# Kernel optimization log

Measured on AMD Instinct MI355X. Metric: run time of the kernel, lower is better.

Reference implementation:

```python
import jax, jax.numpy as jnp
import numpy as np

N_HEADS = 4
M = 16            # n_points (neighbors kept per voxel)
DIST = 4          # manhattan distance threshold
D_MODEL = 128
D_FFN = 256
D_CHL = 64
GRID = 96         # spatial_shape per axis
LN_EPS = 1e-5
BN_EPS = 1e-3


def setup_inputs() -> dict:
    key = jax.random.key(0)
    ks = jax.random.split(key, 24)
    N = 8192
    w = lambda k, s: jax.random.normal(k, s, jnp.float32) * 0.02
    z = lambda d: jnp.zeros((d,), jnp.float32)
    o = lambda d: jnp.ones((d,), jnp.float32)
    return {
        "features": jax.random.normal(ks[0], (N, D_CHL), jnp.float32),
        "coords": jax.random.randint(ks[1], (N, 3), 0, GRID, jnp.int32),
        "pe_w1": w(ks[2], (3, D_MODEL // 2)), "pe_b1": z(D_MODEL // 2),
        "pe_w2": w(ks[3], (D_MODEL // 2, D_MODEL)), "pe_b2": z(D_MODEL),
        "in_w": w(ks[4], (D_CHL, D_MODEL)), "in_b": z(D_MODEL),
        "q_w": w(ks[5], (D_MODEL, D_MODEL)), "q_b": z(D_MODEL),
        "k_w": w(ks[6], (D_MODEL, D_MODEL)), "k_b": z(D_MODEL),
        "v_w": w(ks[7], (D_MODEL, D_MODEL)), "v_b": z(D_MODEL),
        "o_w": w(ks[8], (D_MODEL, D_MODEL)), "o_b": z(D_MODEL),
        "n1_g": o(D_MODEL), "n1_b": z(D_MODEL),
        "l1_w": w(ks[9], (D_MODEL, D_FFN)), "l1_b": z(D_FFN),
        "l2_w": w(ks[10], (D_FFN, D_MODEL)), "l2_b": z(D_MODEL),
        "n3_g": o(D_MODEL), "n3_b": z(D_MODEL),
        "fu_w": w(ks[11], (D_MODEL + D_CHL, D_CHL)), "fu_b": z(D_CHL),
        "bn_g": o(D_CHL), "bn_b": z(D_CHL),
    }


def _layernorm(x, g, b):
    mu = jnp.mean(x, -1, keepdims=True)
    var = jnp.mean(jnp.square(x - mu), -1, keepdims=True)
    return (x - mu) * jax.lax.rsqrt(var + LN_EPS) * g + b


def reference(features, coords, pe_w1, pe_b1, pe_w2, pe_b2, in_w, in_b,
              q_w, q_b, k_w, k_b, v_w, v_b, o_w, o_b, n1_g, n1_b,
              l1_w, l1_b, l2_w, l2_b, n3_g, n3_b, fu_w, fu_b, bn_g, bn_b):
    N = features.shape[0]
    hd = D_MODEL // N_HEADS
    ci = coords.astype(jnp.float32)
    # input projection + dynamic learnable positional encoding
    src = features @ in_w + in_b
    vc = ci / (GRID - 1.0)
    src = src + (jax.nn.relu(vc @ pe_w1 + pe_b1) @ pe_w2 + pe_b2)
    # pairwise manhattan distances; accumulate per coordinate to avoid [N,N,3]
    dist = jnp.zeros((N, N), jnp.float32)
    for d in range(3):
        dist = dist + jnp.abs(ci[:, d, None] - ci[None, :, d])
    dist = jnp.where(dist <= DIST, dist, jnp.inf)
    neg_top, idx = jax.lax.top_k(-dist, M)          # [N, M]
    valid = neg_top != -jnp.inf
    # gather neighbor features; invalid slots are zero (as in torch)
    nb = jnp.where(valid[:, :, None], src[jnp.where(valid, idx, 0)], 0.0)  # [N,M,D]
    # cross-attention: query is neighbor 0 (self). NOTE: faithful raw .view
    # reshape of [N,M,D] -> [N,H,M,hd] (interleaves neighbor/head axes as torch does)
    q = (nb[:, :1] @ q_w + q_b).reshape(N, N_HEADS, 1, hd)
    k = (nb @ k_w + k_b).reshape(N, N_HEADS, M, hd)
    v = (nb @ v_w + v_b).reshape(N, N_HEADS, M, hd)
    scores = jnp.einsum('nhqd,nhkd->nhqk', q, k) / jnp.sqrt(jnp.float32(D_MODEL))
    attn = jax.nn.softmax(scores, axis=-1)
    head_out = jnp.einsum('nhqk,nhkd->nhqd', attn, v).reshape(N, D_MODEL)
    out = head_out @ o_w + o_b
    tgt = _layernorm(src + out, n1_g, n1_b)
    # FFN
    tgt2 = jax.nn.relu(tgt @ l1_w + l1_b) @ l2_w + l2_b
    tgt = _layernorm(tgt + tgt2, n3_g, n3_b)
    # EnhancedFusion: concat -> linear -> batchnorm (train-mode stats) -> relu
    fused = jnp.concatenate([features, tgt], axis=1) @ fu_w + fu_b
    mu = jnp.mean(fused, 0)
    var = jnp.var(fused, 0)
    fused = (fused - mu) * jax.lax.rsqrt(var + BN_EPS) * bn_g + bn_b
    return jax.nn.relu(fused)
```

## Files before the change

### kernel.cpp

```cpp
#include <hip/hip_runtime.h>

#define DEVFN __device__ __forceinline__

DEVFN float relu(float x) { return x < 0.f ? 0.f : x; }

__global__ __launch_bounds__(256, 4) void ka_pre_cst(
    const float* __restrict__ features, const int* __restrict__ coords,
    const float* __restrict__ pe_w1, const float* __restrict__ pe_b1,
    const float* __restrict__ pe_w2, const float* __restrict__ pe_b2,
    const float* __restrict__ in_w, const float* __restrict__ in_b,
    const float* __restrict__ q_w, const float* __restrict__ k_w,
    const float* __restrict__ v_w,
    float* __restrict__ src,
    float* __restrict__ qs, float* __restrict__ ks, float* __restrict__ vs,
    int* __restrict__ nbr, float* __restrict__ bnAcc, int N)
{
    __shared__ __align__(16) float sF[512];
    __shared__ __align__(16) float sH[512];
    __shared__ __align__(16) float S[1024];
    __shared__ int   sC[24];
    __shared__ int cnt[16];
    __shared__ int lst[16 * 64];
    __shared__ int outL[256];

    const int tid = threadIdx.x;
    const int bx = blockIdx.x;
    const int role_nbr = (bx % 3) == 2;

    if (role_nbr) {
        const int nb = bx / 3;
        const int q0 = nb * 16;
        if (nb == 0 && tid < 128) bnAcc[tid] = 0.f;
        if (tid < 16) cnt[tid] = 0;
        outL[tid] = -1;
        __syncthreads();
        int qx[16], qy[16], qz[16];
#pragma unroll
        for (int q = 0; q < 16; ++q) {
            qx[q] = coords[(q0 + q) * 3 + 0];
            qy[q] = coords[(q0 + q) * 3 + 1];
            qz[q] = coords[(q0 + q) * 3 + 2];
        }
        for (int cd = tid; cd < N; cd += 256) {
            int cx = coords[cd * 3 + 0];
            int cy = coords[cd * 3 + 1];
            int cz = coords[cd * 3 + 2];
#pragma unroll
            for (int q = 0; q < 16; ++q) {
                int dx = cx - qx[q]; dx = dx < 0 ? -dx : dx;
                int dy = cy - qy[q]; dy = dy < 0 ? -dy : dy;
                int dz = cz - qz[q]; dz = dz < 0 ? -dz : dz;
                int d = dx + dy + dz;
                if (d <= 4) {
                    int s = atomicAdd(&cnt[q], 1);
                    if (s < 64) lst[q * 64 + s] = (d << 13) | cd;
                }
            }
        }
        __syncthreads();
        {
            const int q = tid >> 4, t = tid & 15;
            int n = cnt[q]; if (n > 64) n = 64;
            for (int e = t; e < n; e += 16) {
                int key = lst[q * 64 + e];
                int rank = 0;
                for (int j = 0; j < n; ++j) rank += (lst[q * 64 + j] < key) ? 1 : 0;
                if (rank < 16) outL[q * 16 + rank] = key & 8191;
            }
        }
        __syncthreads();
        {
            const int q = tid >> 4, t = tid & 15;
            nbr[(q0 + q) * 16 + t] = outL[q * 16 + t];
        }
        return;
    }

    const int sb = (bx / 3) * 2 + (bx % 3);
    const int r0 = sb * 8;
    if (tid < 24) sC[tid] = coords[r0 * 3 + tid];
    for (int i = tid; i < 512; i += 256) sF[i] = features[r0 * 64 + i];
    __syncthreads();
    for (int i = tid; i < 512; i += 256) {
        int r = i >> 6, t = i & 63;
        float v0 = sC[r * 3 + 0] * (1.f / 95.f);
        float v1 = sC[r * 3 + 1] * (1.f / 95.f);
        float v2 = sC[r * 3 + 2] * (1.f / 95.f);
        float h = v0 * pe_w1[t] + v1 * pe_w1[64 + t] + v2 * pe_w1[128 + t] + pe_b1[t];
        sH[i] = relu(h);
    }
    __syncthreads();
    const int c = tid & 127, rh = tid >> 7;
    {
        float acc[4];
        const float base = in_b[c] + pe_b2[c];
#pragma unroll
        for (int r = 0; r < 4; ++r) acc[r] = base;
        const float* wi = in_w + c;
        const float* wp = pe_w2 + c;
        float i0 = wi[0 * 128], i1 = wi[1 * 128], i2 = wi[2 * 128], i3 = wi[3 * 128];
        float p0 = wp[0 * 128], p1 = wp[1 * 128], p2 = wp[2 * 128], p3 = wp[3 * 128];
        for (int j4 = 0; j4 < 16; ++j4) {
            const int jn = ((j4 + 1) & 15) * 4;
            float ni0 = wi[(jn + 0) * 128], ni1 = wi[(jn + 1) * 128];
            float ni2 = wi[(jn + 2) * 128], ni3 = wi[(jn + 3) * 128];
            float np0 = wp[(jn + 0) * 128], np1 = wp[(jn + 1) * 128];
            float np2 = wp[(jn + 2) * 128], np3 = wp[(jn + 3) * 128];
#pragma unroll
            for (int r = 0; r < 4; ++r) {
                const int rr = rh * 4 + r;
                float4 f = *(const float4*)(&sF[rr * 64 + j4 * 4]);
                float4 h = *(const float4*)(&sH[rr * 64 + j4 * 4]);
                acc[r] += f.x * i0 + f.y * i1 + f.z * i2 + f.w * i3
                        + h.x * p0 + h.y * p1 + h.z * p2 + h.w * p3;
            }
            i0 = ni0; i1 = ni1; i2 = ni2; i3 = ni3;
            p0 = np0; p1 = np1; p2 = np2; p3 = np3;
        }
#pragma unroll
        for (int r = 0; r < 4; ++r) {
            src[(r0 + rh * 4 + r) * 128 + c] = acc[r];
            S[(rh * 4 + r) * 128 + c] = acc[r];
        }
    }
    __syncthreads();
    {
        float aq[4], ak[4], av[4];
#pragma unroll
        for (int r = 0; r < 4; ++r) { aq[r] = 0.f; ak[r] = 0.f; av[r] = 0.f; }
        const float* wq = q_w + c;
        const float* wk = k_w + c;
        const float* wv = v_w + c;
        float q0 = wq[0 * 128], q1 = wq[1 * 128], q2 = wq[2 * 128], q3 = wq[3 * 128];
        float k0 = wk[0 * 128], k1 = wk[1 * 128], k2 = wk[2 * 128], k3 = wk[3 * 128];
        float v0 = wv[0 * 128], v1 = wv[1 * 128], v2 = wv[2 * 128], v3 = wv[3 * 128];
        for (int k4 = 0; k4 < 32; ++k4) {
            const int kn = ((k4 + 1) & 31) * 4;
            float nq0 = wq[(kn + 0) * 128], nq1 = wq[(kn + 1) * 128];
            float nq2 = wq[(kn + 2) * 128], nq3 = wq[(kn + 3) * 128];
            float nk0 = wk[(kn + 0) * 128], nk1 = wk[(kn + 1) * 128];
            float nk2 = wk[(kn + 2) * 128], nk3 = wk[(kn + 3) * 128];
            float nv0 = wv[(kn + 0) * 128], nv1 = wv[(kn + 1) * 128];
            float nv2 = wv[(kn + 2) * 128], nv3 = wv[(kn + 3) * 128];
#pragma unroll
            for (int r = 0; r < 4; ++r) {
                float4 s = *(const float4*)(&S[(rh * 4 + r) * 128 + k4 * 4]);
                aq[r] += s.x * q0 + s.y * q1 + s.z * q2 + s.w * q3;
                ak[r] += s.x * k0 + s.y * k1 + s.z * k2 + s.w * k3;
                av[r] += s.x * v0 + s.y * v1 + s.z * v2 + s.w * v3;
            }
            q0 = nq0; q1 = nq1; q2 = nq2; q3 = nq3;
            k0 = nk0; k1 = nk1; k2 = nk2; k3 = nk3;
            v0 = nv0; v1 = nv1; v2 = nv2; v3 = nv3;
        }
#pragma unroll
        for (int r = 0; r < 4; ++r) {
            qs[(r0 + rh * 4 + r) * 128 + c] = aq[r];
            ks[(r0 + rh * 4 + r) * 128 + c] = ak[r];
            vs[(r0 + rh * 4 + r) * 128 + c] = av[r];
        }
    }
}

DEVFN void ln_rows8(float* Cb, const float* __restrict__ g,
                    const float* __restrict__ b, int tid)
{
    const int r = tid >> 5, l = tid & 31;
    float x[4]; float s = 0.f, s2 = 0.f;
#pragma unroll
    for (int i = 0; i < 4; ++i) {
        x[i] = Cb[r * 128 + l * 4 + i];
        s += x[i]; s2 += x[i] * x[i];
    }
#pragma unroll
    for (int o = 1; o < 32; o <<= 1) { s += __shfl_xor(s, o); s2 += __shfl_xor(s2, o); }
    float mu = s * (1.f / 128.f);
    float var = s2 * (1.f / 128.f) - mu * mu;
    float rstd = rsqrtf(var + 1e-5f);
#pragma unroll
    for (int i = 0; i < 4; ++i) {
        int cc = l * 4 + i;
        Cb[r * 128 + cc] = (x[i] - mu) * rstd * g[cc] + b[cc];
    }
}

__global__ __launch_bounds__(256, 4) void k4_main_cst(
    const float* __restrict__ features, const float* __restrict__ src,
    const float* __restrict__ qs, const float* __restrict__ ks, const float* __restrict__ vs,
    const int* __restrict__ nbr,
    const float* __restrict__ q_b, const float* __restrict__ k_b,
    const float* __restrict__ v_b,
    const float* __restrict__ o_w, const float* __restrict__ o_b,
    const float* __restrict__ n1_g, const float* __restrict__ n1_b,
    const float* __restrict__ l1_w, const float* __restrict__ l1_b,
    const float* __restrict__ l2_w, const float* __restrict__ l2_b,
    const float* __restrict__ n3_g, const float* __restrict__ n3_b,
    const float* __restrict__ fu_w, const float* __restrict__ fu_b,
    float* __restrict__ fused, float* __restrict__ bnSum, float* __restrict__ bnSq)
{
    __shared__ __align__(16) float A[1024];
    __shared__ __align__(16) float Bt[1024];
    __shared__ __align__(16) float C[1024];
    __shared__ __align__(16) float Q[1024];
    __shared__ __align__(16) float H[2048];
    __shared__ __align__(16) float SC[512];
    __shared__ __align__(16) float F[512];
    __shared__ __align__(16) float bK[128], bV[128];
    __shared__ int idxL[128];
    const int tid = threadIdx.x;
    const int r0 = blockIdx.x * 8;

    for (int i = tid; i < 1024; i += 256) A[i] = src[r0 * 128 + i];
    for (int i = tid; i < 512; i += 256) F[i] = features[r0 * 64 + i];
    if (tid < 128) {
        idxL[tid] = nbr[r0 * 16 + tid];
        bK[tid] = k_b[tid]; bV[tid] = v_b[tid];
    }
    __syncthreads();
    {
        int r = tid >> 5, cg = tid & 31;
        int i0 = idxL[r * 16];
        float4 qv = make_float4(0.f, 0.f, 0.f, 0.f);
        if (i0 >= 0) qv = *(const float4*)(qs + i0 * 128 + cg * 4);
        float4 qb = *(const float4*)(q_b + cg * 4);
        qv.x += qb.x; qv.y += qb.y; qv.z += qb.z; qv.w += qb.w;
        *(float4*)(&Q[r * 128 + cg * 4]) = qv;
    }
    __syncthreads();

    const int ar = tid >> 5, ah = (tid >> 3) & 3, ag = tid & 7;
    {
#pragma unroll
        for (int jj = 0; jj < 2; ++jj) {
            int j = ag + jj * 8;
            int j4 = j >> 2, ch = j & 3;
            int id = idxL[ar * 16 + ah * 4 + j4];
            float s = 0.f;
#pragma unroll
            for (int c4 = 0; c4 < 8; ++c4) {
                float4 qv = *(const float4*)(&Q[ar * 128 + ah * 32 + c4 * 4]);
                float4 kb = *(const float4*)(&bK[ch * 32 + c4 * 4]);
                float4 kv = make_float4(0.f, 0.f, 0.f, 0.f);
                if (id >= 0) kv = *(const float4*)(ks + id * 128 + ch * 32 + c4 * 4);
                s += qv.x * (kv.x + kb.x) + qv.y * (kv.y + kb.y)
                   + qv.z * (kv.z + kb.z) + qv.w * (kv.w + kb.w);
            }
            SC[ar * 64 + ah * 16 + j] = s * 0.08838834764831845f;
        }
    }
    __syncthreads();

    {
        float p[16];
        float mx = -3.4e38f;
#pragma unroll
        for (int j = 0; j < 16; ++j) { p[j] = SC[ar * 64 + ah * 16 + j]; mx = fmaxf(mx, p[j]); }
        float sum = 0.f;
#pragma unroll
        for (int j = 0; j < 16; ++j) { p[j] = __expf(p[j] - mx); sum += p[j]; }
        float inv = 1.f / sum;
        float4 acc = make_float4(0.f, 0.f, 0.f, 0.f);
#pragma unroll
        for (int j = 0; j < 16; ++j) {
            int j4 = j >> 2, ch = j & 3;
            int id = idxL[ar * 16 + ah * 4 + j4];
            float4 vb = *(const float4*)(&bV[ch * 32 + ag * 4]);
            float4 vv = make_float4(0.f, 0.f, 0.f, 0.f);
            if (id >= 0) vv = *(const float4*)(vs + id * 128 + ch * 32 + ag * 4);
            float w = p[j] * inv;
            acc.x += w * (vv.x + vb.x); acc.y += w * (vv.y + vb.y);
            acc.z += w * (vv.z + vb.z); acc.w += w * (vv.w + vb.w);
        }
        *(float4*)(&Bt[ar * 128 + ah * 32 + ag * 4]) = acc;
    }
    __syncthreads();

    {
        const int c = tid & 127, kh = tid >> 7;
        float acc[8];
#pragma unroll
        for (int r = 0; r < 8; ++r) acc[r] = 0.f;
        const float* wp = o_w + kh * 64 * 128 + c;
        float w0 = wp[0 * 128], w1 = wp[1 * 128], w2 = wp[2 * 128], w3 = wp[3 * 128];
        for (int k4 = 0; k4 < 16; ++k4) {
            const int kn = ((k4 + 1) & 15) * 4;
            float n0 = wp[(kn + 0) * 128], n1 = wp[(kn + 1) * 128];
            float n2 = wp[(kn + 2) * 128], n3 = wp[(kn + 3) * 128];
#pragma unroll
            for (int r = 0; r < 8; ++r) {
                float4 t = *(const float4*)(&Bt[r * 128 + kh * 64 + k4 * 4]);
                acc[r] += t.x * w0 + t.y * w1 + t.z * w2 + t.w * w3;
            }
            w0 = n0; w1 = n1; w2 = n2; w3 = n3;
        }
#pragma unroll
        for (int r = 0; r < 8; ++r) H[kh * 1024 + r * 128 + c] = acc[r];
    }
    __syncthreads();
    for (int i = tid; i < 1024; i += 256) {
        int c = i & 127;
        C[i] = A[i] + o_b[c] + H[i] + H[1024 + i];
    }
    __syncthreads();
    ln_rows8(C, n1_g, n1_b, tid);
    __syncthreads();

    {
        const int f = tid;
        float acc[8];
#pragma unroll
        for (int r = 0; r < 8; ++r) acc[r] = 0.f;
        const float* wp = l1_w + f;
        float w0 = wp[0 * 256], w1 = wp[1 * 256], w2 = wp[2 * 256], w3 = wp[3 * 256];
        for (int k4 = 0; k4 < 32; ++k4) {
            const int kn = ((k4 + 1) & 31) * 4;
            float n0 = wp[(kn + 0) * 256], n1 = wp[(kn + 1) * 256];
            float n2 = wp[(kn + 2) * 256], n3 = wp[(kn + 3) * 256];
#pragma unroll
            for (int r = 0; r < 8; ++r) {
                float4 t = *(const float4*)(&C[r * 128 + k4 * 4]);
                acc[r] += t.x * w0 + t.y * w1 + t.z * w2 + t.w * w3;
            }
            w0 = n0; w1 = n1; w2 = n2; w3 = n3;
        }
        const float bb = l1_b[f];
#pragma unroll
        for (int r = 0; r < 8; ++r) H[r * 256 + f] = relu(acc[r] + bb);
    }
    __syncthreads();

    {
        const int c = tid & 127, kh = tid >> 7;
        float acc[8];
#pragma unroll
        for (int r = 0; r < 8; ++r) acc[r] = 0.f;
        const float* wp = l2_w + kh * 128 * 128 + c;
        float w0 = wp[0 * 128], w1 = wp[1 * 128], w2 = wp[2 * 128], w3 = wp[3 * 128];
        for (int k4 = 0; k4 < 32; ++k4) {
            const int kn = ((k4 + 1) & 31) * 4;
            float n0 = wp[(kn + 0) * 128], n1 = wp[(kn + 1) * 128];
            float n2 = wp[(kn + 2) * 128], n3 = wp[(kn + 3) * 128];
#pragma unroll
            for (int r = 0; r < 8; ++r) {
                float4 t = *(const float4*)(&H[r * 256 + kh * 128 + k4 * 4]);
                acc[r] += t.x * w0 + t.y * w1 + t.z * w2 + t.w * w3;
            }
            w0 = n0; w1 = n1; w2 = n2; w3 = n3;
        }
        float* P = kh ? Bt : A;
#pragma unroll
        for (int r = 0; r < 8; ++r) P[r * 128 + c] = acc[r];
    }
    __syncthreads();
    for (int i = tid; i < 1024; i += 256) {
        int c = i & 127;
        C[i] += l2_b[c] + A[i] + Bt[i];
    }
    __syncthreads();
    ln_rows8(C, n3_g, n3_b, tid);
    __syncthreads();

    {
        const int c = tid & 63, rg = tid >> 6;
        float acc[2];
        const float fb = fu_b[c];
#pragma unroll
        for (int r = 0; r < 2; ++r) acc[r] = fb;
        const float* wA = fu_w + c;
        float w0 = wA[0 * 64], w1 = wA[1 * 64], w2 = wA[2 * 64], w3 = wA[3 * 64];
        for (int j4 = 0; j4 < 16; ++j4) {
            const int jn = ((j4 + 1) & 15) * 4;
            float n0 = wA[(jn + 0) * 64], n1 = wA[(jn + 1) * 64];
            float n2 = wA[(jn + 2) * 64], n3 = wA[(jn + 3) * 64];
#pragma unroll
            for (int r = 0; r < 2; ++r) {
                float4 t = *(const float4*)(&F[(rg * 2 + r) * 64 + j4 * 4]);
                acc[r] += t.x * w0 + t.y * w1 + t.z * w2 + t.w * w3;
            }
            w0 = n0; w1 = n1; w2 = n2; w3 = n3;
        }
        const float* wB = fu_w + 64 * 64 + c;
        w0 = wB[0 * 64]; w1 = wB[1 * 64]; w2 = wB[2 * 64]; w3 = wB[3 * 64];
        for (int j4 = 0; j4 < 32; ++j4) {
            const int jn = ((j4 + 1) & 31) * 4;
            float n0 = wB[(jn + 0) * 64], n1 = wB[(jn + 1) * 64];
            float n2 = wB[(jn + 2) * 64], n3 = wB[(jn + 3) * 64];
#pragma unroll
            for (int r = 0; r < 2; ++r) {
                float4 t = *(const float4*)(&C[(rg * 2 + r) * 128 + j4 * 4]);
                acc[r] += t.x * w0 + t.y * w1 + t.z * w2 + t.w * w3;
            }
            w0 = n0; w1 = n1; w2 = n2; w3 = n3;
        }
#pragma unroll
        for (int r = 0; r < 2; ++r) {
            int row = rg * 2 + r;
            float v = acc[r];
            fused[(r0 + row) * 64 + c] = v;
            H[row * 64 + c] = v;
        }
    }
    __syncthreads();
    if (tid < 64) {
        float s = 0.f, s2 = 0.f;
#pragma unroll
        for (int r = 0; r < 8; ++r) { float x = H[r * 64 + tid]; s += x; s2 += x * x; }
        atomicAdd(&bnSum[tid], s);
        atomicAdd(&bnSq[tid], s2);
    }
}

__global__ __launch_bounds__(256) void k5_bn_cst(
    const float* __restrict__ fused, const float* __restrict__ bnSum,
    const float* __restrict__ bnSq,
    const float* __restrict__ g, const float* __restrict__ b,
    float* __restrict__ out, int N)
{
    const int total = N * 64;
    const float invN = 1.f / (float)N;
    for (int i = blockIdx.x * 256 + threadIdx.x; i < total; i += gridDim.x * 256) {
        int c = i & 63;
        float mu = bnSum[c] * invN;
        float var = bnSq[c] * invN - mu * mu;
        float x = fused[i];
        float y = (x - mu) * rsqrtf(var + 1e-3f) * g[c] + b[c];
        out[i] = relu(y);
    }
}

extern "C" void kernel_launch(void* const* d_in, const int* in_sizes, int n_in,
                              void* d_out, int out_size, void* d_ws, size_t ws_size,
                              hipStream_t stream)
{
    const float* features = (const float*)d_in[0];
    const int*   coords   = (const int*)d_in[1];
    const float* pe_w1 = (const float*)d_in[2];
    const float* pe_b1 = (const float*)d_in[3];
    const float* pe_w2 = (const float*)d_in[4];
    const float* pe_b2 = (const float*)d_in[5];
    const float* in_w  = (const float*)d_in[6];
    const float* in_b  = (const float*)d_in[7];
    const float* q_w   = (const float*)d_in[8];
    const float* q_b   = (const float*)d_in[9];
    const float* k_w   = (const float*)d_in[10];
    const float* k_b   = (const float*)d_in[11];
    const float* v_w   = (const float*)d_in[12];
    const float* v_b   = (const float*)d_in[13];
    const float* o_w   = (const float*)d_in[14];
    const float* o_b   = (const float*)d_in[15];
    const float* n1_g  = (const float*)d_in[16];
    const float* n1_b  = (const float*)d_in[17];
    const float* l1_w  = (const float*)d_in[18];
    const float* l1_b  = (const float*)d_in[19];
    const float* l2_w  = (const float*)d_in[20];
    const float* l2_b  = (const float*)d_in[21];
    const float* n3_g  = (const float*)d_in[22];
    const float* n3_b  = (const float*)d_in[23];
    const float* fu_w  = (const float*)d_in[24];
    const float* fu_b  = (const float*)d_in[25];
    const float* bn_g  = (const float*)d_in[26];
    const float* bn_b  = (const float*)d_in[27];

    const int N = in_sizes[0] / 64;

    float* src   = (float*)d_ws;
    float* qs    = src + (size_t)N * 128;
    float* ks    = qs  + (size_t)N * 128;
    float* vs    = ks  + (size_t)N * 128;
    float* fused = vs  + (size_t)N * 128;
    int*   nbr    = (int*)(fused + (size_t)N * 64);
    float* bnSum  = (float*)(nbr + (size_t)N * 16);
    float* bnSq   = bnSum + 64;

    ka_pre_cst<<<N / 8 + N / 16, 256, 0, stream>>>(features, coords,
                                                   pe_w1, pe_b1, pe_w2, pe_b2,
                                                   in_w, in_b, q_w, k_w, v_w,
                                                   src, qs, ks, vs, nbr, bnSum, N);
    k4_main_cst<<<N / 8, 256, 0, stream>>>(features, src, qs, ks, vs, nbr,
                                           q_b, k_b, v_b, o_w, o_b, n1_g, n1_b,
                                           l1_w, l1_b, l2_w, l2_b, n3_g, n3_b,
                                           fu_w, fu_b, fused, bnSum, bnSq);
    k5_bn_cst<<<512, 256, 0, stream>>>(fused, bnSum, bnSq, bn_g, bn_b,
                                       (float*)d_out, N);
}
```

Before: 229.7 us.

## Retile dense GEMM stages with split-K register blocking and vectorized weight loads

Restructures the QKV projection, output projection, and both FFN matmuls so each thread computes a small 4-row by 2-4-column register tile over a slice of the K dimension. Partial sums are combined through shared memory, and weights are fetched with float2/float4 vector loads. This is meant to cut per-FLOP global weight traffic and raise arithmetic intensity per thread. It also drops the manual software prefetch of weights in the remaining loops. In exchange it adds extra shared memory (a larger H buffer and new partial-sum buffers) plus extra barriers, which may lower occupancy.

```diff
diff --git a/kernel.cpp b/kernel.cpp
--- a/kernel.cpp
+++ b/kernel.cpp
@@ -18,6 +18,9 @@
     __shared__ __align__(16) float sF[512];
     __shared__ __align__(16) float sH[512];
     __shared__ __align__(16) float S[1024];
+    __shared__ __align__(16) float sQP[1024];
+    __shared__ __align__(16) float sKP[1024];
+    __shared__ __align__(16) float sVP[1024];
     __shared__ int   sC[24];
     __shared__ int cnt[16];
     __shared__ int lst[16 * 64];
@@ -90,22 +93,19 @@
         sH[i] = relu(h);
     }
     __syncthreads();
-    const int c = tid & 127, rh = tid >> 7;
-    {
+    {
+        const int c = tid & 127, rh = tid >> 7;
         float acc[4];
         const float base = in_b[c] + pe_b2[c];
 #pragma unroll
         for (int r = 0; r < 4; ++r) acc[r] = base;
         const float* wi = in_w + c;
         const float* wp = pe_w2 + c;
-        float i0 = wi[0 * 128], i1 = wi[1 * 128], i2 = wi[2 * 128], i3 = wi[3 * 128];
-        float p0 = wp[0 * 128], p1 = wp[1 * 128], p2 = wp[2 * 128], p3 = wp[3 * 128];
         for (int j4 = 0; j4 < 16; ++j4) {
-            const int jn = ((j4 + 1) & 15) * 4;
-            float ni0 = wi[(jn + 0) * 128], ni1 = wi[(jn + 1) * 128];
-            float ni2 = wi[(jn + 2) * 128], ni3 = wi[(jn + 3) * 128];
-            float np0 = wp[(jn + 0) * 128], np1 = wp[(jn + 1) * 128];
-            float np2 = wp[(jn + 2) * 128], np3 = wp[(jn + 3) * 128];
+            float i0 = wi[(j4 * 4 + 0) * 128], i1 = wi[(j4 * 4 + 1) * 128];
+            float i2 = wi[(j4 * 4 + 2) * 128], i3 = wi[(j4 * 4 + 3) * 128];
+            float p0 = wp[(j4 * 4 + 0) * 128], p1 = wp[(j4 * 4 + 1) * 128];
+            float p2 = wp[(j4 * 4 + 2) * 128], p3 = wp[(j4 * 4 + 3) * 128];
 #pragma unroll
             for (int r = 0; r < 4; ++r) {
                 const int rr = rh * 4 + r;
@@ -114,8 +114,6 @@
                 acc[r] += f.x * i0 + f.y * i1 + f.z * i2 + f.w * i3
                         + h.x * p0 + h.y * p1 + h.z * p2 + h.w * p3;
             }
-            i0 = ni0; i1 = ni1; i2 = ni2; i3 = ni3;
-            p0 = np0; p1 = np1; p2 = np2; p3 = np3;
         }
 #pragma unroll
         for (int r = 0; r < 4; ++r) {
@@ -125,39 +123,54 @@
     }
     __syncthreads();
     {
-        float aq[4], ak[4], av[4];
-#pragma unroll
-        for (int r = 0; r < 4; ++r) { aq[r] = 0.f; ak[r] = 0.f; av[r] = 0.f; }
-        const float* wq = q_w + c;
-        const float* wk = k_w + c;
-        const float* wv = v_w + c;
-        float q0 = wq[0 * 128], q1 = wq[1 * 128], q2 = wq[2 * 128], q3 = wq[3 * 128];
-        float k0 = wk[0 * 128], k1 = wk[1 * 128], k2 = wk[2 * 128], k3 = wk[3 * 128];
-        float v0 = wv[0 * 128], v1 = wv[1 * 128], v2 = wv[2 * 128], v3 = wv[3 * 128];
-        for (int k4 = 0; k4 < 32; ++k4) {
-            const int kn = ((k4 + 1) & 31) * 4;
-            float nq0 = wq[(kn + 0) * 128], nq1 = wq[(kn + 1) * 128];
-            float nq2 = wq[(kn + 2) * 128], nq3 = wq[(kn + 3) * 128];
-            float nk0 = wk[(kn + 0) * 128], nk1 = wk[(kn + 1) * 128];
-            float nk2 = wk[(kn + 2) * 128], nk3 = wk[(kn + 3) * 128];
-            float nv0 = wv[(kn + 0) * 128], nv1 = wv[(kn + 1) * 128];
-            float nv2 = wv[(kn + 2) * 128], nv3 = wv[(kn + 3) * 128];
-#pragma unroll
-            for (int r = 0; r < 4; ++r) {
-                float4 s = *(const float4*)(&S[(rh * 4 + r) * 128 + k4 * 4]);
-                aq[r] += s.x * q0 + s.y * q1 + s.z * q2 + s.w * q3;
-                ak[r] += s.x * k0 + s.y * k1 + s.z * k2 + s.w * k3;
-                av[r] += s.x * v0 + s.y * v1 + s.z * v2 + s.w * v3;
-            }
-            q0 = nq0; q1 = nq1; q2 = nq2; q3 = nq3;
-            k0 = nk0; k1 = nk1; k2 = nk2; k3 = nk3;
-            v0 = nv0; v1 = nv1; v2 = nv2; v3 = nv3;
-        }
-#pragma unroll
-        for (int r = 0; r < 4; ++r) {
-            qs[(r0 + rh * 4 + r) * 128 + c] = aq[r];
-            ks[(r0 + rh * 4 + r) * 128 + c] = ak[r];
-            vs[(r0 + rh * 4 + r) * 128 + c] = av[r];
+        const int cp = tid & 63, rh2 = (tid >> 6) & 1, kh = tid >> 7;
+        const int c0 = cp * 2, r0l = rh2 * 4, k0 = kh * 64;
+        float aq[4][2], ak[4][2], av[4][2];
+#pragma unroll
+        for (int r = 0; r < 4; ++r)
+            for (int cc = 0; cc < 2; ++cc) { aq[r][cc] = 0.f; ak[r][cc] = 0.f; av[r][cc] = 0.f; }
+        for (int s = 0; s < 16; ++s) {
+            const int kk = k0 + s * 4;
+            float2 wq[4], wk[4], wv[4];
+#pragma unroll
+            for (int j = 0; j < 4; ++j) {
+                wq[j] = *(const float2*)(q_w + (kk + j) * 128 + c0);
+                wk[j] = *(const float2*)(k_w + (kk + j) * 128 + c0);
+                wv[j] = *(const float2*)(v_w + (kk + j) * 128 + c0);
+            }
+#pragma unroll
+            for (int r = 0; r < 4; ++r) {
+                float4 s4 = *(const float4*)(&S[(r0l + r) * 128 + kk]);
+                aq[r][0] += s4.x * wq[0].x + s4.y * wq[1].x + s4.z * wq[2].x + s4.w * wq[3].x;
+                aq[r][1] += s4.x * wq[0].y + s4.y * wq[1].y + s4.z * wq[2].y + s4.w * wq[3].y;
+                ak[r][0] += s4.x * wk[0].x + s4.y * wk[1].x + s4.z * wk[2].x + s4.w * wk[3].x;
+                ak[r][1] += s4.x * wk[0].y + s4.y * wk[1].y + s4.z * wk[2].y + s4.w * wk[3].y;
+                av[r][0] += s4.x * wv[0].x + s4.y * wv[1].x + s4.z * wv[2].x + s4.w * wv[3].x;
+                av[r][1] += s4.x * wv[0].y + s4.y * wv[1].y + s4.z * wv[2].y + s4.w * wv[3].y;
+            }
+        }
+        if (kh) {
+#pragma unroll
+            for (int r = 0; r < 4; ++r) {
+                const int base = (r0l + r) * 128 + c0;
+                *(float2*)(&sQP[base]) = make_float2(aq[r][0], aq[r][1]);
+                *(float2*)(&sKP[base]) = make_float2(ak[r][0], ak[r][1]);
+                *(float2*)(&sVP[base]) = make_float2(av[r][0], av[r][1]);
+            }
+        }
+        __syncthreads();
+        if (kh == 0) {
+#pragma unroll
+            for (int r = 0; r < 4; ++r) {
+                const int base = (r0l + r) * 128 + c0;
+                const int g = (r0 + r0l + r) * 128 + c0;
+                float2 pq = *(const float2*)(&sQP[base]);
+                float2 pk = *(const float2*)(&sKP[base]);
+                float2 pv = *(const float2*)(&sVP[base]);
+                *(float2*)(qs + g) = make_float2(aq[r][0] + pq.x, aq[r][1] + pq.y);
+                *(float2*)(ks + g) = make_float2(ak[r][0] + pk.x, ak[r][1] + pk.y);
+                *(float2*)(vs + g) = make_float2(av[r][0] + pv.x, av[r][1] + pv.y);
+            }
         }
     }
 }
@@ -202,7 +215,7 @@
     __shared__ __align__(16) float Bt[1024];
     __shared__ __align__(16) float C[1024];
     __shared__ __align__(16) float Q[1024];
-    __shared__ __align__(16) float H[2048];
+    __shared__ __align__(16) float H[3072];
     __shared__ __align__(16) float SC[512];
     __shared__ __align__(16) float F[512];
     __shared__ __align__(16) float bK[128], bV[128];
@@ -276,87 +289,148 @@
     __syncthreads();
 
     {
-        const int c = tid & 127, kh = tid >> 7;
-        float acc[8];
-#pragma unroll
-        for (int r = 0; r < 8; ++r) acc[r] = 0.f;
-        const float* wp = o_w + kh * 64 * 128 + c;
-        float w0 = wp[0 * 128], w1 = wp[1 * 128], w2 = wp[2 * 128], w3 = wp[3 * 128];
-        for (int k4 = 0; k4 < 16; ++k4) {
-            const int kn = ((k4 + 1) & 15) * 4;
-            float n0 = wp[(kn + 0) * 128], n1 = wp[(kn + 1) * 128];
-            float n2 = wp[(kn + 2) * 128], n3 = wp[(kn + 3) * 128];
-#pragma unroll
-            for (int r = 0; r < 8; ++r) {
-                float4 t = *(const float4*)(&Bt[r * 128 + kh * 64 + k4 * 4]);
-                acc[r] += t.x * w0 + t.y * w1 + t.z * w2 + t.w * w3;
-            }
-            w0 = n0; w1 = n1; w2 = n2; w3 = n3;
-        }
-#pragma unroll
-        for (int r = 0; r < 8; ++r) H[kh * 1024 + r * 128 + c] = acc[r];
-    }
-    __syncthreads();
-    for (int i = tid; i < 1024; i += 256) {
-        int c = i & 127;
-        C[i] = A[i] + o_b[c] + H[i] + H[1024 + i];
-    }
-    __syncthreads();
+        const int cg = tid & 31, rg = (tid >> 5) & 1, kh = tid >> 6;
+        const int c0 = cg * 4, r0l = rg * 4, k0 = kh * 32;
+        float acc[4][4];
+#pragma unroll
+        for (int r = 0; r < 4; ++r)
+            for (int cc = 0; cc < 4; ++cc) acc[r][cc] = 0.f;
+        for (int s = 0; s < 8; ++s) {
+            const int kk = k0 + s * 4;
+            float4 w[4];
+#pragma unroll
+            for (int j = 0; j < 4; ++j) w[j] = *(const float4*)(o_w + (kk + j) * 128 + c0);
+#pragma unroll
+            for (int r = 0; r < 4; ++r) {
+                float4 a = *(const float4*)(&Bt[(r0l + r) * 128 + kk]);
+                acc[r][0] += a.x * w[0].x + a.y * w[1].x + a.z * w[2].x + a.w * w[3].x;
+                acc[r][1] += a.x * w[0].y + a.y * w[1].y + a.z * w[2].y + a.w * w[3].y;
+                acc[r][2] += a.x * w[0].z + a.y * w[1].z + a.z * w[2].z + a.w * w[3].z;
+                acc[r][3] += a.x * w[0].w + a.y * w[1].w + a.z * w[2].w + a.w * w[3].w;
+            }
+        }
+        if (kh) {
+            float* dst = &H[(kh - 1) * 1024];
+#pragma unroll
+            for (int r = 0; r < 4; ++r)
+                *(float4*)(&dst[(r0l + r) * 128 + c0]) =
+                    make_float4(acc[r][0], acc[r][1], acc[r][2], acc[r][3]);
+        }
+        __syncthreads();
+        if (kh == 0) {
+            float4 ob = *(const float4*)(o_b + c0);
+#pragma unroll
+            for (int r = 0; r < 4; ++r) {
+                const int base = (r0l + r) * 128 + c0;
+                float4 av = *(const float4*)(&A[base]);
+                float4 p0 = *(const float4*)(&H[base]);
+                float4 p1 = *(const float4*)(&H[1024 + base]);
+                float4 p2 = *(const float4*)(&H[2048 + base]);
+                float4 cv;
+                cv.x = av.x + ob.x + acc[r][0] + p0.x + p1.x + p2.x;
+                cv.y = av.y + ob.y + acc[r][1] + p0.y + p1.y + p2.y;
+                cv.z = av.z + ob.z + acc[r][2] + p0.z + p1.z + p2.z;
+                cv.w = av.w + ob.w + acc[r][3] + p0.w + p1.w + p2.w;
+                *(float4*)(&C[base]) = cv;
+            }
+        }
+        __syncthreads();
+    }
     ln_rows8(C, n1_g, n1_b, tid);
     __syncthreads();
 
     {
-        const int f = tid;
-        float acc[8];
-#pragma unroll
-        for (int r = 0; r < 8; ++r) acc[r] = 0.f;
-        const float* wp = l1_w + f;
-        float w0 = wp[0 * 256], w1 = wp[1 * 256], w2 = wp[2 * 256], w3 = wp[3 * 256];
-        for (int k4 = 0; k4 < 32; ++k4) {
-            const int kn = ((k4 + 1) & 31) * 4;
-            float n0 = wp[(kn + 0) * 256], n1 = wp[(kn + 1) * 256];
-            float n2 = wp[(kn + 2) * 256], n3 = wp[(kn + 3) * 256];
-#pragma unroll
-            for (int r = 0; r < 8; ++r) {
-                float4 t = *(const float4*)(&C[r * 128 + k4 * 4]);
-                acc[r] += t.x * w0 + t.y * w1 + t.z * w2 + t.w * w3;
-            }
-            w0 = n0; w1 = n1; w2 = n2; w3 = n3;
-        }
-        const float bb = l1_b[f];
-#pragma unroll
-        for (int r = 0; r < 8; ++r) H[r * 256 + f] = relu(acc[r] + bb);
-    }
-    __syncthreads();
-
-    {
-        const int c = tid & 127, kh = tid >> 7;
-        float acc[8];
-#pragma unroll
-        for (int r = 0; r < 8; ++r) acc[r] = 0.f;
-        const float* wp = l2_w + kh * 128 * 128 + c;
-        float w0 = wp[0 * 128], w1 = wp[1 * 128], w2 = wp[2 * 128], w3 = wp[3 * 128];
-        for (int k4 = 0; k4 < 32; ++k4) {
-            const int kn = ((k4 + 1) & 31) * 4;
-            float n0 = wp[(kn + 0) * 128], n1 = wp[(kn + 1) * 128];
-            float n2 = wp[(kn + 2) * 128], n3 = wp[(kn + 3) * 128];
-#pragma unroll
-            for (int r = 0; r < 8; ++r) {
-                float4 t = *(const float4*)(&H[r * 256 + kh * 128 + k4 * 4]);
-                acc[r] += t.x * w0 + t.y * w1 + t.z * w2 + t.w * w3;
-            }
-            w0 = n0; w1 = n1; w2 = n2; w3 = n3;
-        }
-        float* P = kh ? Bt : A;
-#pragma unroll
-        for (int r = 0; r < 8; ++r) P[r * 128 + c] = acc[r];
-    }
-    __syncthreads();
-    for (int i = tid; i < 1024; i += 256) {
-        int c = i & 127;
-        C[i] += l2_b[c] + A[i] + Bt[i];
-    }
-    __syncthreads();
+        const int cg = tid & 63, rg = (tid >> 6) & 1, kh = tid >> 7;
+        const int c0 = cg * 4, r0l = rg * 4, k0 = kh * 64;
+        float acc[4][4];
+#pragma unroll
+        for (int r = 0; r < 4; ++r)
+            for (int cc = 0; cc < 4; ++cc) acc[r][cc] = 0.f;
+        for (int s = 0; s < 16; ++s) {
+            const int kk = k0 + s * 4;
+            float4 w[4];
+#pragma unroll
+            for (int j = 0; j < 4; ++j) w[j] = *(const float4*)(l1_w + (kk + j) * 256 + c0);
+#pragma unroll
+            for (int r = 0; r < 4; ++r) {
+                float4 a = *(const float4*)(&C[(r0l + r) * 128 + kk]);
+                acc[r][0] += a.x * w[0].x + a.y * w[1].x + a.z * w[2].x + a.w * w[3].x;
+                acc[r][1] += a.x * w[0].y + a.y * w[1].y + a.z * w[2].y + a.w * w[3].y;
+                acc[r][2] += a.x * w[0].z + a.y * w[1].z + a.z * w[2].z + a.w * w[3].z;
+                acc[r][3] += a.x * w[0].w + a.y * w[1].w + a.z * w[2].w + a.w * w[3].w;
+            }
+        }
+        float* PS = rg ? Bt : A;
+        if (kh) {
+#pragma unroll
+            for (int r = 0; r < 4; ++r)
+                *(float4*)(&PS[r * 256 + c0]) =
+                    make_float4(acc[r][0], acc[r][1], acc[r][2], acc[r][3]);
+        }
+        __syncthreads();
+        if (kh == 0) {
+            float4 lb = *(const float4*)(l1_b + c0);
+#pragma unroll
+            for (int r = 0; r < 4; ++r) {
+                float4 p = *(const float4*)(&PS[r * 256 + c0]);
+                float4 h;
+                h.x = relu(acc[r][0] + p.x + lb.x);
+                h.y = relu(acc[r][1] + p.y + lb.y);
+                h.z = relu(acc[r][2] + p.z + lb.z);
+                h.w = relu(acc[r][3] + p.w + lb.w);
+                *(float4*)(&H[(r0l + r) * 256 + c0]) = h;
+            }
+        }
+        __syncthreads();
+    }
+
+    {
+        const int cg = tid & 31, rg = (tid >> 5) & 1, kh = tid >> 6;
+        const int c0 = cg * 4, r0l = rg * 4, k0 = kh * 64;
+        float acc[4][4];
+#pragma unroll
+        for (int r = 0; r < 4; ++r)
+            for (int cc = 0; cc < 4; ++cc) acc[r][cc] = 0.f;
+        for (int s = 0; s < 16; ++s) {
+            const int kk = k0 + s * 4;
+            float4 w[4];
+#pragma unroll
+            for (int j = 0; j < 4; ++j) w[j] = *(const float4*)(l2_w + (kk + j) * 128 + c0);
+#pragma unroll
+            for (int r = 0; r < 4; ++r) {
+                float4 a = *(const float4*)(&H[(r0l + r) * 256 + kk]);
+                acc[r][0] += a.x * w[0].x + a.y * w[1].x + a.z * w[2].x + a.w * w[3].x;
+                acc[r][1] += a.x * w[0].y + a.y * w[1].y + a.z * w[2].y + a.w * w[3].y;
+                acc[r][2] += a.x * w[0].z + a.y * w[1].z + a.z * w[2].z + a.w * w[3].z;
+                acc[r][3] += a.x * w[0].w + a.y * w[1].w + a.z * w[2].w + a.w * w[3].w;
+            }
+        }
+        if (kh) {
+            float* dst = (kh == 1) ? A : ((kh == 2) ? Bt : Q);
+#pragma unroll
+            for (int r = 0; r < 4; ++r)
+                *(float4*)(&dst[(r0l + r) * 128 + c0]) =
+                    make_float4(acc[r][0], acc[r][1], acc[r][2], acc[r][3]);
+        }
+        __syncthreads();
+        if (kh == 0) {
+            float4 lb = *(const float4*)(l2_b + c0);
+#pragma unroll
+            for (int r = 0; r < 4; ++r) {
+                const int base = (r0l + r) * 128 + c0;
+                float4 cv = *(const float4*)(&C[base]);
+                float4 p0 = *(const float4*)(&A[base]);
+                float4 p1 = *(const float4*)(&Bt[base]);
+                float4 p2 = *(const float4*)(&Q[base]);
+                cv.x += lb.x + acc[r][0] + p0.x + p1.x + p2.x;
+                cv.y += lb.y + acc[r][1] + p0.y + p1.y + p2.y;
+                cv.z += lb.z + acc[r][2] + p0.z + p1.z + p2.z;
+                cv.w += lb.w + acc[r][3] + p0.w + p1.w + p2.w;
+                *(float4*)(&C[base]) = cv;
+            }
+        }
+        __syncthreads();
+    }
     ln_rows8(C, n3_g, n3_b, tid);
     __syncthreads();
 
@@ -367,30 +441,24 @@
 #pragma unroll
         for (int r = 0; r < 2; ++r) acc[r] = fb;
         const float* wA = fu_w + c;
-        float w0 = wA[0 * 64], w1 = wA[1 * 64], w2 = wA[2 * 64], w3 = wA[3 * 64];
         for (int j4 = 0; j4 < 16; ++j4) {
-            const int jn = ((j4 + 1) & 15) * 4;
-            float n0 = wA[(jn + 0) * 64], n1 = wA[(jn + 1) * 64];
-            float n2 = wA[(jn + 2) * 64], n3 = wA[(jn + 3) * 64];
+            float w0 = wA[(j4 * 4 + 0) * 64], w1 = wA[(j4 * 4 + 1) * 64];
+            float w2 = wA[(j4 * 4 + 2) * 64], w3 = wA[(j4 * 4 + 3) * 64];
 #pragma unroll
             for (int r = 0; r < 2; ++r) {
                 float4 t = *(const float4*)(&F[(rg * 2 + r) * 64 + j4 * 4]);
                 acc[r] += t.x * w0 + t.y * w1 + t.z * w2 + t.w * w3;
             }
-            w0 = n0; w1 = n1; w2 = n2; w3 = n3;
         }
         const float* wB = fu_w + 64 * 64 + c;
-        w0 = wB[0 * 64]; w1 = wB[1 * 64]; w2 = wB[2 * 64]; w3 = wB[3 * 64];
         for (int j4 = 0; j4 < 32; ++j4) {
-            const int jn = ((j4 + 1) & 31) * 4;
-            float n0 = wB[(jn + 0) * 64], n1 = wB[(jn + 1) * 64];
-            float n2 = wB[(jn + 2) * 64], n3 = wB[(jn + 3) * 64];
+            float w0 = wB[(j4 * 4 + 0) * 64], w1 = wB[(j4 * 4 + 1) * 64];
+            float w2 = wB[(j4 * 4 + 2) * 64], w3 = wB[(j4 * 4 + 3) * 64];
 #pragma unroll
             for (int r = 0; r < 2; ++r) {
                 float4 t = *(const float4*)(&C[(rg * 2 + r) * 128 + j4 * 4]);
                 acc[r] += t.x * w0 + t.y * w1 + t.z * w2 + t.w * w3;
             }
-            w0 = n0; w1 = n1; w2 = n2; w3 = n3;
         }
 #pragma unroll
         for (int r = 0; r < 2; ++r) {
```

After: 358.5 us. 56.0% more time.
